# Optimization experiments

Hardware: AMD Instinct MI355X
Metric: run time of the kernel (lower is better)

## Reference

```python
import jax, jax.numpy as jnp
import numpy as np

SCALE = 2
GROUPS = 4

def _up_axis(x, axis, s):
    # torch F.interpolate bilinear, align_corners=False, along one axis
    n = x.shape[axis]
    src = jnp.maximum((jnp.arange(n * s, dtype=jnp.float32) + 0.5) / s - 0.5, 0.0)
    i0 = jnp.minimum(jnp.floor(src).astype(jnp.int32), n - 1)
    i1 = jnp.minimum(i0 + 1, n - 1)
    t = (src - i0.astype(jnp.float32)).astype(x.dtype)
    shp = [1] * x.ndim
    shp[axis] = -1
    t = t.reshape(shp)
    return jnp.take(x, i0, axis=axis) * (1 - t) + jnp.take(x, i1, axis=axis) * t

def _grid_sample(img, grid):
    # img: (N,C,H,W); grid: (N,Hg,Wg,2) xy in [-1,1]; bilinear, align_corners=False, zeros padding
    N, C, H, W = img.shape
    gx = (grid[..., 0] + 1.0) * (W * 0.5) - 0.5
    gy = (grid[..., 1] + 1.0) * (H * 0.5) - 0.5
    x0 = jnp.floor(gx)
    y0 = jnp.floor(gy)
    tx = (gx - x0).astype(img.dtype)
    ty = (gy - y0).astype(img.dtype)
    x0 = x0.astype(jnp.int32)
    y0 = y0.astype(jnp.int32)
    flat = img.reshape(N, C, H * W)

    def corner(xi, yi, wgt):
        valid = ((xi >= 0) & (xi < W) & (yi >= 0) & (yi < H)).astype(img.dtype)
        idx = (jnp.clip(yi, 0, H - 1) * W + jnp.clip(xi, 0, W - 1)).reshape(N, -1)
        v = jax.vmap(lambda f, i: f[:, i])(flat, idx)  # (N,C,P) irregular gather
        return v * (wgt * valid).reshape(N, 1, -1)

    out = (corner(x0, y0, (1 - tx) * (1 - ty))
           + corner(x0 + 1, y0, tx * (1 - ty))
           + corner(x0, y0 + 1, (1 - tx) * ty)
           + corner(x0 + 1, y0 + 1, tx * ty))
    return out.reshape(N, C, grid.shape[1], grid.shape[2])

def _forward(x, w_off, b_off, w_mask, b_mask):
    s, g = SCALE, GROUPS
    b, c, h, w = x.shape
    # 1x1 convs
    offset = jnp.einsum('bchw,oc->bohw', x, w_off) + b_off[None, :, None, None]  # (b,2g,h,w)
    mask = jax.nn.sigmoid(jnp.einsum('bchw,gc->bghw', x, w_mask) + b_mask[None, :, None, None])  # (b,g,h,w)
    # bilinear upsample then split into s*s subpixel feature maps (one per group)
    x_up = _up_axis(_up_axis(x, 2, s), 3, s)  # (b,c,s*h,s*w)
    feat = x_up.reshape(b, c, s, h, s, w).transpose(0, 2, 4, 1, 3, 5).reshape(b, s * s, c, h, w)[:, :g]
    # per-group offset-perturbed sampling coordinates
    off = offset.reshape(b, g, 2, h, w).transpose(0, 1, 3, 4, 2)  # (b,g,h,w,2) (x,y)
    gy, gx = jnp.meshgrid(jnp.arange(h, dtype=x.dtype), jnp.arange(w, dtype=x.dtype), indexing='ij')
    base = jnp.stack([gx, gy], axis=-1)  # (h,w,2)
    coords = base[None, None] + off
    norm = (coords / jnp.array([w, h], dtype=x.dtype) - 0.5) * 2.0
    sampled = _grid_sample(feat.reshape(b * g, c, h, w), norm.reshape(b * g, h, w, 2))
    sampled = sampled.reshape(b, g, c, h, w)
    # sigmoid-mask weighting and group-sum reduction
    return (sampled * mask[:, :, None]).sum(axis=1)  # (b,c,h,w)

def setup_inputs():
    key = jax.random.key(0)
    k1, k2, k3, k4, k5 = jax.random.split(key, 5)
    b, c, h, w, g = 16, 64, 128, 128, GROUPS
    return {
        'x': jax.random.normal(k1, (b, c, h, w), jnp.float32),
        'w_off': jax.random.normal(k2, (2 * g, c), jnp.float32) * 0.1,
        'b_off': jax.random.normal(k3, (2 * g,), jnp.float32) * 0.1,
        'w_mask': jax.random.normal(k4, (g, c), jnp.float32) * 0.1,
        'b_mask': jax.random.normal(k5, (g,), jnp.float32) * 0.1,
    }

def reference(x, w_off, b_off, w_mask, b_mask):
    return _forward(x, w_off, b_off, w_mask, b_mask)
```

## Files before the change

### kernel.cpp

```cpp
#include <hip/hip_runtime.h>
#include <hip/hip_fp16.h>

#define CC 64
#define HH 128
#define WW 128
#define HWS (HH * WW)
#define NG 4

__device__ __forceinline__ void make_taps(float gp, int n, int half, int& base,
                                          float& w0o, float& w1o, float& w2o) {
  float w0 = 0.0f, w1 = 0.0f, w2 = 0.0f;
  float f = floorf(gp);
  int x0 = (int)f;
  float t = gp - f;
  int b = 0;
#pragma unroll
  for (int k = 0; k < 2; ++k) {
    int xc = x0 + k;
    float cw = k ? t : 1.0f - t;
    if (xc < 0 || xc >= n) cw = 0.0f;
    int xcc = min(max(xc, 0), n - 1);
    int u = half * n + xcc;
    float src = fmaxf((float)u * 0.5f - 0.25f, 0.0f);
    float sf = floorf(src);
    int i0 = (int)sf;
    float tu = src - sf;
    int i1 = min(i0 + 1, n - 1);
    if (k == 0) b = i0;
    int s0 = i0 - b;
    int s1 = i1 - b;
    float a0 = cw * (1.0f - tu);
    float a1 = cw * tu;
    w0 += (s0 == 0) ? a0 : 0.0f;
    w1 += (s0 == 1) ? a0 : 0.0f;
    w0 += (s1 == 0) ? a1 : 0.0f;
    w1 += (s1 == 1) ? a1 : 0.0f;
    w2 += (s1 == 2) ? a1 : 0.0f;
  }
  base = b;
  w0o = w0; w1o = w1; w2o = w2;
}

__global__ __launch_bounds__(256) void prep_v3(
    const float* __restrict__ x,
    const float* __restrict__ w_off, const float* __restrict__ b_off,
    const float* __restrict__ w_mask, const float* __restrict__ b_mask,
    __half* __restrict__ xT, float* __restrict__ geomC, int npix) {
  __shared__ float wt[CC * 12];
  __shared__ unsigned int tile[64][33];
  __shared__ float part[4][64][13];
  int t = threadIdx.x;
  for (int idx = t; idx < CC * 12; idx += 256) {
    int c = idx / 12, d = idx - c * 12;
    wt[idx] = (d < 8) ? w_off[d * CC + c] : w_mask[(d - 8) * CC + c];
  }
  __syncthreads();

  int px = t & 63, chq = t >> 6;
  int pix = blockIdx.x * 64 + px;
  int b = pix >> 14;
  int ij = pix & (HWS - 1);
  const float* __restrict__ xp = x + (size_t)b * CC * HWS + ij;

  float xv[16];
#pragma unroll
  for (int k = 0; k < 16; ++k) xv[k] = xp[(size_t)(chq * 16 + k) * HWS];

  float p12[12];
#pragma unroll
  for (int d = 0; d < 12; ++d) p12[d] = 0.0f;
#pragma unroll
  for (int k = 0; k < 16; ++k) {
    int c = chq * 16 + k;
    float v = xv[k];
    const float4 w0 = *reinterpret_cast<const float4*>(&wt[c * 12 + 0]);
    const float4 w1 = *reinterpret_cast<const float4*>(&wt[c * 12 + 4]);
    const float4 w2 = *reinterpret_cast<const float4*>(&wt[c * 12 + 8]);
    p12[0]  = fmaf(w0.x, v, p12[0]);   p12[1]  = fmaf(w0.y, v, p12[1]);
    p12[2]  = fmaf(w0.z, v, p12[2]);   p12[3]  = fmaf(w0.w, v, p12[3]);
    p12[4]  = fmaf(w1.x, v, p12[4]);   p12[5]  = fmaf(w1.y, v, p12[5]);
    p12[6]  = fmaf(w1.z, v, p12[6]);   p12[7]  = fmaf(w1.w, v, p12[7]);
    p12[8]  = fmaf(w2.x, v, p12[8]);   p12[9]  = fmaf(w2.y, v, p12[9]);
    p12[10] = fmaf(w2.z, v, p12[10]);  p12[11] = fmaf(w2.w, v, p12[11]);
  }

#pragma unroll
  for (int k = 0; k < 8; ++k) {
    tile[px][chq * 8 + k] = __builtin_bit_cast(
        unsigned int, __floats2half2_rn(xv[2 * k], xv[2 * k + 1]));
  }
#pragma unroll
  for (int d = 0; d < 12; ++d) part[chq][px][d] = p12[d];
  __syncthreads();

  {
    unsigned int* __restrict__ xtu = reinterpret_cast<unsigned int*>(xT);
    size_t base = (size_t)blockIdx.x * 64 * 32;
    int spx = t >> 2, c0 = (t & 3) * 8;
    uint4 u0, u1;
    u0.x = tile[spx][c0 + 0]; u0.y = tile[spx][c0 + 1];
    u0.z = tile[spx][c0 + 2]; u0.w = tile[spx][c0 + 3];
    u1.x = tile[spx][c0 + 4]; u1.y = tile[spx][c0 + 5];
    u1.z = tile[spx][c0 + 6]; u1.w = tile[spx][c0 + 7];
    *reinterpret_cast<uint4*>(xtu + base + t * 8) = u0;
    *reinterpret_cast<uint4*>(xtu + base + t * 8 + 4) = u1;
  }

  if (t < 64) {
    int pixg = blockIdx.x * 64 + t;
    int ijg = pixg & (HWS - 1);
    int i = ijg >> 7, j = ijg & (WW - 1);
    float a12[12];
#pragma unroll
    for (int d = 0; d < 12; ++d) {
      a12[d] = ((d < 8) ? b_off[d] : b_mask[d - 8]) + part[0][t][d] +
               part[1][t][d] + part[2][t][d] + part[3][t][d];
    }
    float* __restrict__ gb = geomC + (size_t)(pixg >> 5) * 1024 + (pixg & 31);
#pragma unroll
    for (int g = 0; g < NG; ++g) {
      int sy = g >> 1, sx = g & 1;
      float mg = 1.0f / (1.0f + __expf(-a12[8 + g]));
      int cb, rb;
      float x0, x1, x2, y0, y1, y2;
      make_taps((float)j + a12[2 * g]     - 0.5f, WW, sx, cb, x0, x1, x2);
      make_taps((float)i + a12[2 * g + 1] - 0.5f, HH, sy, rb, y0, y1, y2);
      gb[(g * 8 + 0) * 32] = x0;
      gb[(g * 8 + 1) * 32] = x1;
      gb[(g * 8 + 2) * 32] = x2;
      gb[(g * 8 + 3) * 32] = y0 * mg;
      gb[(g * 8 + 4) * 32] = y1 * mg;
      gb[(g * 8 + 5) * 32] = y2 * mg;
      gb[(g * 8 + 6) * 32] = __int_as_float(rb);
      gb[(g * 8 + 7) * 32] = __int_as_float(cb);
    }
  }
}

__global__ __launch_bounds__(256) void sample16(
    const __half* __restrict__ xT, const float* __restrict__ geomC,
    float* __restrict__ out, int npix) {
  __shared__ float graw[1024];
  __shared__ int2 gexp[32][36];
  int t = threadIdx.x;

  int nwg = gridDim.x, bid = blockIdx.x;
  int swz = ((nwg & 7) == 0) ? ((bid & 7) * (nwg >> 3) + (bid >> 3)) : bid;

  reinterpret_cast<uint4*>(graw)[t] =
      reinterpret_cast<const uint4*>(geomC + (size_t)swz * 1024)[t];
  __syncthreads();

  if (t < 128) {
    int p = t >> 2, g = t & 3;
    float wx0 = graw[(g * 8 + 0) * 32 + p];
    float wx1 = graw[(g * 8 + 1) * 32 + p];
    float wx2 = graw[(g * 8 + 2) * 32 + p];
    float wy0 = graw[(g * 8 + 3) * 32 + p];
    float wy1 = graw[(g * 8 + 4) * 32 + p];
    float wy2 = graw[(g * 8 + 5) * 32 + p];
    int rb = __float_as_int(graw[(g * 8 + 6) * 32 + p]);
    int cb = __float_as_int(graw[(g * 8 + 7) * 32 + p]);
#pragma unroll
    for (int dy = 0; dy < 3; ++dy) {
      int ro = min(rb + dy, HH - 1) * WW;
      float wyv = (dy == 0) ? wy0 : ((dy == 1) ? wy1 : wy2);
#pragma unroll
      for (int dx = 0; dx < 3; ++dx) {
        int off = ro + min(cb + dx, WW - 1);
        float wv = wyv * ((dx == 0) ? wx0 : ((dx == 1) ? wx1 : wx2));
        gexp[p][g * 9 + dy * 3 + dx] =
            make_int2(off, __builtin_bit_cast(int, __float2half2_rn(wv)));
      }
    }
  }
  __syncthreads();

  int p = t >> 3, r = t & 7;
  int pix = swz * 32 + p;
  int b = pix >> 14, ij = pix & (HWS - 1);
  const __half* __restrict__ xb = xT + ((size_t)b * HWS) * 64 + r * 8;

  __half2 acc0 = __float2half2_rn(0.0f);
  __half2 acc1 = acc0, acc2 = acc0, acc3 = acc0;

#pragma unroll
  for (int k = 0; k < 36; ++k) {
    int2 ow = gexp[p][k];
    __half2 wh = __builtin_bit_cast(__half2, ow.y);
    uint4 v = *reinterpret_cast<const uint4*>(xb + (size_t)ow.x * 64);
    acc0 = __hfma2(__builtin_bit_cast(__half2, v.x), wh, acc0);
    acc1 = __hfma2(__builtin_bit_cast(__half2, v.y), wh, acc1);
    acc2 = __hfma2(__builtin_bit_cast(__half2, v.z), wh, acc2);
    acc3 = __hfma2(__builtin_bit_cast(__half2, v.w), wh, acc3);
  }

  float2 f0 = __half22float2(acc0);
  float2 f1 = __half22float2(acc1);
  float2 f2 = __half22float2(acc2);
  float2 f3 = __half22float2(acc3);
  float* __restrict__ op = out + ((size_t)b * CC + r * 8) * HWS + ij;
  op[0 * HWS] = f0.x;  op[1 * HWS] = f0.y;
  op[2 * HWS] = f1.x;  op[3 * HWS] = f1.y;
  op[4 * HWS] = f2.x;  op[5 * HWS] = f2.y;
  op[6 * HWS] = f3.x;  op[7 * HWS] = f3.y;
}

__global__ __launch_bounds__(256) void dysample_fused(
    const float* __restrict__ x,
    const float* __restrict__ w_off, const float* __restrict__ b_off,
    const float* __restrict__ w_mask, const float* __restrict__ b_mask,
    float* __restrict__ out, int npix) {
  __shared__ float wt[CC * 12];
  for (int idx = threadIdx.x; idx < CC * 12; idx += 256) {
    int c = idx / 12, d = idx - c * 12;
    wt[idx] = (d < 8) ? w_off[d * CC + c] : w_mask[(d - 8) * CC + c];
  }
  __syncthreads();
  int nwg = gridDim.x;
  int bid = blockIdx.x;
  int swz = ((nwg & 7) == 0) ? ((bid & 7) * (nwg >> 3) + (bid >> 3)) : bid;
  int pix = swz * 256 + threadIdx.x;
  if (pix >= npix) return;
  int b = pix >> 14;
  int ij = pix & (HWS - 1);
  int i = ij >> 7, j = ij & (WW - 1);
  const float* __restrict__ xp = x + (size_t)b * CC * HWS;
  float a12[12];
#pragma unroll
  for (int d = 0; d < 12; ++d) a12[d] = (d < 8) ? b_off[d] : b_mask[d - 8];
#pragma unroll 4
  for (int c = 0; c < CC; ++c) {
    float xv = xp[c * HWS + ij];
    const float4 w0 = *reinterpret_cast<const float4*>(&wt[c * 12 + 0]);
    const float4 w1 = *reinterpret_cast<const float4*>(&wt[c * 12 + 4]);
    const float4 w2 = *reinterpret_cast<const float4*>(&wt[c * 12 + 8]);
    a12[0]  = fmaf(w0.x, xv, a12[0]);   a12[1]  = fmaf(w0.y, xv, a12[1]);
    a12[2]  = fmaf(w0.z, xv, a12[2]);   a12[3]  = fmaf(w0.w, xv, a12[3]);
    a12[4]  = fmaf(w1.x, xv, a12[4]);   a12[5]  = fmaf(w1.y, xv, a12[5]);
    a12[6]  = fmaf(w1.z, xv, a12[6]);   a12[7]  = fmaf(w1.w, xv, a12[7]);
    a12[8]  = fmaf(w2.x, xv, a12[8]);   a12[9]  = fmaf(w2.y, xv, a12[9]);
    a12[10] = fmaf(w2.z, xv, a12[10]);  a12[11] = fmaf(w2.w, xv, a12[11]);
  }
  int ro[NG][3], co[NG][3];
  float wx[NG][3], wy[NG][3];
#pragma unroll
  for (int g = 0; g < NG; ++g) {
    int sy = g >> 1, sx = g & 1;
    float mg = 1.0f / (1.0f + __expf(-a12[8 + g]));
    int cb, rb;
    float x0, x1, x2, y0, y1, y2;
    make_taps((float)j + a12[2 * g]     - 0.5f, WW, sx, cb, x0, x1, x2);
    make_taps((float)i + a12[2 * g + 1] - 0.5f, HH, sy, rb, y0, y1, y2);
    wx[g][0] = x0;      wx[g][1] = x1;      wx[g][2] = x2;
    wy[g][0] = y0 * mg; wy[g][1] = y1 * mg; wy[g][2] = y2 * mg;
#pragma unroll
    for (int d = 0; d < 3; ++d) {
      ro[g][d] = min(rb + d, HH - 1) * WW;
      co[g][d] = min(cb + d, WW - 1);
    }
  }
  float* __restrict__ op = out + (size_t)b * CC * HWS + ij;
  for (int blk = 0; blk < 4; ++blk) {
    const float* __restrict__ xb = xp + blk * 16 * HWS;
    float acc[16];
#pragma unroll
    for (int c = 0; c < 16; ++c) acc[c] = 0.0f;
#pragma unroll
    for (int g = 0; g < NG; ++g) {
      int o9[9];
      float w9[9];
#pragma unroll
      for (int dy = 0; dy < 3; ++dy) {
#pragma unroll
        for (int dx = 0; dx < 3; ++dx) {
          o9[dy * 3 + dx] = ro[g][dy] + co[g][dx];
          w9[dy * 3 + dx] = wy[g][dy] * wx[g][dx];
        }
      }
#pragma unroll
      for (int c = 0; c < 16; ++c) {
        const float* __restrict__ xc = xb + c * HWS;
#pragma unroll
        for (int k = 0; k < 9; ++k) acc[c] = fmaf(w9[k], xc[o9[k]], acc[c]);
      }
    }
#pragma unroll
    for (int c = 0; c < 16; ++c) op[(blk * 16 + c) * HWS] = acc[c];
  }
}

extern "C" void kernel_launch(void* const* d_in, const int* in_sizes, int n_in,
                              void* d_out, int out_size, void* d_ws, size_t ws_size,
                              hipStream_t stream) {
  const float* x      = (const float*)d_in[0];
  const float* w_off  = (const float*)d_in[1];
  const float* b_off  = (const float*)d_in[2];
  const float* w_mask = (const float*)d_in[3];
  const float* b_mask = (const float*)d_in[4];
  float* out = (float*)d_out;

  int B = in_sizes[0] / (CC * HWS);
  int npix = B * HWS;
  size_t need = (size_t)npix * 128 + (size_t)npix * 128;

  if (ws_size >= need && (npix & 255) == 0) {
    __half* xT   = (__half*)d_ws;
    float* geomC = (float*)((char*)d_ws + (size_t)npix * 128);
    hipLaunchKernelGGL(prep_v3, dim3(npix / 64), dim3(256), 0, stream,
                       x, w_off, b_off, w_mask, b_mask, xT, geomC, npix);
    hipLaunchKernelGGL(sample16, dim3(npix / 32), dim3(256), 0, stream,
                       xT, geomC, out, npix);
  } else {
    int nblk = (npix + 255) / 256;
    hipLaunchKernelGGL(dysample_fused, dim3(nblk), dim3(256), 0, stream,
                       x, w_off, b_off, w_mask, b_mask, out, npix);
  }
}
```

Measured before the change: 82.63 us.

## Compact zero-weight taps and sort pixels by tap count to shorten gather loop

Each pixel's tap list is compacted so that only taps with nonzero x and y weights are stored, and a per-pixel count is recorded. Pixels are then ranked by tap count so each 64-lane wave covers pixels with similar counts, and the gather loop runs only to the longest count in its wave instead of a fixed 36. This aims to cut wasted 16-byte gathers and FMAs for zero-weight taps, at the cost of extra shared memory, two more barriers, a small serial rank sort, and losing full unrolling of the main loop.

```diff
diff --git a/kernel.cpp b/kernel.cpp
--- a/kernel.cpp
+++ b/kernel.cpp
@@ -141,7 +141,10 @@
     const __half* __restrict__ xT, const float* __restrict__ geomC,
     float* __restrict__ out, int npix) {
   __shared__ float graw[1024];
-  __shared__ int2 gexp[32][36];
+  __shared__ int2 gexp[32][38];
+  __shared__ int lens[32][4];
+  __shared__ int lenTotal[32];
+  __shared__ int perm32[32];
   int t = threadIdx.x;
 
   int nwg = gridDim.x, bid = blockIdx.x;
@@ -149,6 +152,20 @@
 
   reinterpret_cast<uint4*>(graw)[t] =
       reinterpret_cast<const uint4*>(geomC + (size_t)swz * 1024)[t];
+  __syncthreads();
+
+  if (t < 128) {
+    int p = t >> 2, g = t & 3;
+    float wx0 = graw[(g * 8 + 0) * 32 + p];
+    float wx1 = graw[(g * 8 + 1) * 32 + p];
+    float wx2 = graw[(g * 8 + 2) * 32 + p];
+    float wy0 = graw[(g * 8 + 3) * 32 + p];
+    float wy1 = graw[(g * 8 + 4) * 32 + p];
+    float wy2 = graw[(g * 8 + 5) * 32 + p];
+    int cx = (wx0 != 0.0f) + (wx1 != 0.0f) + (wx2 != 0.0f);
+    int cy = (wy0 != 0.0f) + (wy1 != 0.0f) + (wy2 != 0.0f);
+    lens[p][g] = cy * cx;
+  }
   __syncthreads();
 
   if (t < 128) {
@@ -161,22 +178,43 @@
     float wy2 = graw[(g * 8 + 5) * 32 + p];
     int rb = __float_as_int(graw[(g * 8 + 6) * 32 + p]);
     int cb = __float_as_int(graw[(g * 8 + 7) * 32 + p]);
+    int c = (g > 0 ? lens[p][0] : 0) + (g > 1 ? lens[p][1] : 0) +
+            (g > 2 ? lens[p][2] : 0);
 #pragma unroll
     for (int dy = 0; dy < 3; ++dy) {
-      int ro = min(rb + dy, HH - 1) * WW;
       float wyv = (dy == 0) ? wy0 : ((dy == 1) ? wy1 : wy2);
-#pragma unroll
-      for (int dx = 0; dx < 3; ++dx) {
-        int off = ro + min(cb + dx, WW - 1);
-        float wv = wyv * ((dx == 0) ? wx0 : ((dx == 1) ? wx1 : wx2));
-        gexp[p][g * 9 + dy * 3 + dx] =
-            make_int2(off, __builtin_bit_cast(int, __float2half2_rn(wv)));
+      if (wyv != 0.0f) {
+        int ro = min(rb + dy, HH - 1) * WW;
+#pragma unroll
+        for (int dx = 0; dx < 3; ++dx) {
+          float wxv = (dx == 0) ? wx0 : ((dx == 1) ? wx1 : wx2);
+          if (wxv != 0.0f) {
+            gexp[p][c] = make_int2(
+                ro + min(cb + dx, WW - 1),
+                __builtin_bit_cast(int, __float2half2_rn(wyv * wxv)));
+            ++c;
+          }
+        }
       }
     }
-  }
-  __syncthreads();
-
-  int p = t >> 3, r = t & 7;
+    if (g == 3) {
+      lenTotal[p] = c;
+      for (int k = c; k < 36; ++k) gexp[p][k] = make_int2(0, 0);
+    }
+  }
+  __syncthreads();
+
+  if (t < 32) {
+    int key = lenTotal[t] * 64 + t;
+    int rank = 0;
+    for (int q = 0; q < 32; ++q) rank += (lenTotal[q] * 64 + q) < key;
+    perm32[rank] = t;
+  }
+  __syncthreads();
+
+  int rank = t >> 3, r = t & 7;
+  int p = perm32[rank];
+  int Lmax = lenTotal[perm32[rank | 7]];
   int pix = swz * 32 + p;
   int b = pix >> 14, ij = pix & (HWS - 1);
   const __half* __restrict__ xb = xT + ((size_t)b * HWS) * 64 + r * 8;
@@ -184,8 +222,7 @@
   __half2 acc0 = __float2half2_rn(0.0f);
   __half2 acc1 = acc0, acc2 = acc0, acc3 = acc0;
 
-#pragma unroll
-  for (int k = 0; k < 36; ++k) {
+  for (int k = 0; k < Lmax; ++k) {
     int2 ow = gexp[p][k];
     __half2 wh = __builtin_bit_cast(__half2, ow.y);
     uint4 v = *reinterpret_cast<const uint4*>(xb + (size_t)ow.x * 64);
```

Measured after the change: 83.43 us. About the same (+1.0%).
